# Kernel optimization log

Hardware: AMD Instinct MI355X
Metric: run time of the kernel (lower is better)

The kernel has to match this reference:

```python
import jax, jax.numpy as jnp
import numpy as np

D, d, s, n = 2048, 64, 32, 65536


def setup_inputs() -> dict:
    key = jax.random.key(0)
    k1, k2, k3, k4 = jax.random.split(key, 4)
    c = jax.random.normal(k1, (D, 1), dtype=jnp.float32)
    # torch parametrizations.orthogonal keeps Q.weight orthonormal-column; emulate via QR
    Q_raw = jax.random.normal(k2, (D, d + s), dtype=jnp.float32)
    Q, _ = jnp.linalg.qr(Q_raw)  # (D, d+s) orthonormal columns
    phi = jax.random.normal(k3, (d, n), dtype=jnp.float32)
    theta = jax.random.normal(k4, (d * (d + 1) // 2, s), dtype=jnp.float32)
    return {"c": c, "Q": Q, "phi": phi, "theta": theta}


def calculate_psi(phi):
    # vectorized upper-triangular outer product: rows ordered (0,0),(0,1),...,(0,d-1),(1,1),...
    dd = phi.shape[0]
    ii, jj = jnp.triu_indices(dd)  # matches the torch double loop ordering
    return phi[ii] * phi[jj]  # (d*(d+1)//2, n)


def reference(c, Q, phi, theta):
    psi = calculate_psi(phi)                       # (d(d+1)/2, n)
    quad = theta.T @ psi                           # (s, n)
    z = jnp.concatenate([phi, quad], axis=0)       # (d+s, n)
    return c + Q @ z                               # (D, n)
```

## Files before the change

### kernel.cpp

```cpp
#include <hip/hip_runtime.h>


__global__ __launch_bounds__(128) void quad_kernel(
    const float* __restrict__ phi,
    const float* __restrict__ theta,
    float* __restrict__ quad,
    const int n)
{
    __shared__ float ph[64][128];
    const int tid = threadIdx.x;
    const int colbase = blockIdx.x * 128;
    const int shalf = blockIdx.y;

    #pragma unroll
    for (int t = 0; t < 64; ++t) {
        const int e = t * 128 + tid;
        const int i = e >> 7;
        const int cc = e & 127;
        ph[i][cc] = phi[(size_t)i * n + colbase + cc];
    }
    __syncthreads();

    const float* __restrict__ th = theta + shalf * 16;

    float acc[16];
    #pragma unroll
    for (int ss = 0; ss < 16; ++ss) acc[ss] = 0.f;

    const float* __restrict__ tk = th;
    for (int i = 0; i < 64; ++i) {
        const float pi = ph[i][tid];
        for (int j = i; j < 64; ++j) {
            const float psi = pi * ph[j][tid];
            #pragma unroll
            for (int ss = 0; ss < 16; ++ss)
                acc[ss] = fmaf(tk[ss], psi, acc[ss]);
            tk += 32;
        }
    }

    const int col = colbase + tid;
    #pragma unroll
    for (int ss = 0; ss < 16; ++ss)
        quad[(size_t)(shalf * 16 + ss) * n + col] = acc[ss];
}

__global__ __launch_bounds__(256) void out_kernel(
    const float* __restrict__ cvec,
    const float* __restrict__ Q,
    const float* __restrict__ phi,
    const float* __restrict__ quad,
    float* __restrict__ out,
    const int n)
{
    __shared__ float Qt[96 * 64];
    __shared__ float Zs[96 * 64];
    const int tid = threadIdx.x;
    const int rowbase = blockIdx.x * 64;
    const int colbase = blockIdx.y * 64;

    {
        const int r = tid >> 2;
        const int kg = (tid & 3) * 24;
        const float* qp = Q + (size_t)(rowbase + r) * 96 + kg;
        #pragma unroll
        for (int t = 0; t < 6; ++t) {
            const float4 v = *(const float4*)(qp + t * 4);
            const int k0 = kg + t * 4;
            Qt[(k0 + 0) * 64 + r] = v.x;
            Qt[(k0 + 1) * 64 + r] = v.y;
            Qt[(k0 + 2) * 64 + r] = v.z;
            Qt[(k0 + 3) * 64 + r] = v.w;
        }
    }
    #pragma unroll
    for (int t = 0; t < 6; ++t) {
        const int q = t * 256 + tid;
        const int k = q >> 4;
        const int c4 = (q & 15) * 4;
        const float* src = (k < 64) ? (phi + (size_t)k * n)
                                    : (quad + (size_t)(k - 64) * n);
        *(float4*)&Zs[k * 64 + c4] = *(const float4*)(src + colbase + c4);
    }
    __syncthreads();

    const int cg = tid & 15;
    const int rg = tid >> 4;
    const int c0 = cg * 4;
    const int r0 = rg * 4;

    float acc[16];
    #pragma unroll
    for (int t = 0; t < 16; ++t) acc[t] = 0.f;

    #pragma unroll 8
    for (int k = 0; k < 96; ++k) {
        const float4 a = *(const float4*)&Qt[k * 64 + r0];
        const float4 b = *(const float4*)&Zs[k * 64 + c0];
        acc[0]  = fmaf(a.x, b.x, acc[0]);
        acc[1]  = fmaf(a.x, b.y, acc[1]);
        acc[2]  = fmaf(a.x, b.z, acc[2]);
        acc[3]  = fmaf(a.x, b.w, acc[3]);
        acc[4]  = fmaf(a.y, b.x, acc[4]);
        acc[5]  = fmaf(a.y, b.y, acc[5]);
        acc[6]  = fmaf(a.y, b.z, acc[6]);
        acc[7]  = fmaf(a.y, b.w, acc[7]);
        acc[8]  = fmaf(a.z, b.x, acc[8]);
        acc[9]  = fmaf(a.z, b.y, acc[9]);
        acc[10] = fmaf(a.z, b.z, acc[10]);
        acc[11] = fmaf(a.z, b.w, acc[11]);
        acc[12] = fmaf(a.w, b.x, acc[12]);
        acc[13] = fmaf(a.w, b.y, acc[13]);
        acc[14] = fmaf(a.w, b.z, acc[14]);
        acc[15] = fmaf(a.w, b.w, acc[15]);
    }

    #pragma unroll
    for (int i = 0; i < 4; ++i) {
        const int row = rowbase + r0 + i;
        const float cv = cvec[row];
        float4 v;
        v.x = acc[i * 4 + 0] + cv;
        v.y = acc[i * 4 + 1] + cv;
        v.z = acc[i * 4 + 2] + cv;
        v.w = acc[i * 4 + 3] + cv;
        *(float4*)&out[(size_t)row * n + colbase + c0] = v;
    }
}

extern "C" void kernel_launch(void* const* d_in, const int* in_sizes, int n_in,
                              void* d_out, int out_size, void* d_ws, size_t ws_size,
                              hipStream_t stream) {
    const float* c     = (const float*)d_in[0];
    const float* Q     = (const float*)d_in[1];
    const float* phi   = (const float*)d_in[2];
    const float* theta = (const float*)d_in[3];
    float* out  = (float*)d_out;
    float* quad = (float*)d_ws;

    const int D = in_sizes[0];
    const int n = in_sizes[2] / 64;

    quad_kernel<<<dim3(n / 128, 2), 128, 0, stream>>>(phi, theta, quad, n);
    out_kernel<<<dim3(D / 64, n / 64), 256, 0, stream>>>(c, Q, phi, quad, out, n);
}
```

Before: 1.014 ms.

## Use split-bf16 MFMA for output GEMM with transposed Z layout and async LDS loads

The fp32 FMA GEMM in the output kernel is replaced by bf16 MFMA 16x16x32 instructions using a hi/lo split (three products per pair) to approximate fp32 accuracy. A new prep kernel splits Q into bf16 hi/lo. The quad kernel now writes phi and quad together as a column-major Z in bf16 hi/lo. The output kernel loads its tiles with global_load_lds and uses a larger column tile. This targets the output GEMM's ALU and LDS cost, at the price of extra conversion work, a bigger workspace, and slightly lower precision from dropping the lo*lo term.

```diff
diff --git a/kernel.cpp b/kernel.cpp
--- a/kernel.cpp
+++ b/kernel.cpp
@@ -1,10 +1,45 @@
 #include <hip/hip_runtime.h>
 
+
+typedef short bf16x8 __attribute__((ext_vector_type(8)));
+typedef float f32x4 __attribute__((ext_vector_type(4)));
+typedef unsigned short u16;
+typedef unsigned int u32;
+
+__device__ inline u16 f2bf_rn(float x) {
+    u32 u = __float_as_uint(x);
+    return (u16)((u + 0x7FFFu + ((u >> 16) & 1u)) >> 16);
+}
+__device__ inline float bf2f(u16 h) { return __uint_as_float((u32)h << 16); }
+__device__ inline void bsplit(float x, u16& h, u16& l) {
+    h = f2bf_rn(x);
+    l = f2bf_rn(x - bf2f(h));
+}
+
+__device__ inline void gload_lds16(const void* g, void* l) {
+    __builtin_amdgcn_global_load_lds(
+        (const __attribute__((address_space(1))) void*)g,
+        (__attribute__((address_space(3))) void*)l,
+        16, 0, 0);
+}
+
+__global__ __launch_bounds__(256) void qprep_kernel(
+    const float* __restrict__ Q, u16* __restrict__ qh, u16* __restrict__ ql,
+    const int total)
+{
+    const int e = blockIdx.x * 256 + threadIdx.x;
+    if (e < total) {
+        u16 h, l;
+        bsplit(Q[e], h, l);
+        qh[e] = h;
+        ql[e] = l;
+    }
+}
 
 __global__ __launch_bounds__(128) void quad_kernel(
     const float* __restrict__ phi,
     const float* __restrict__ theta,
-    float* __restrict__ quad,
+    u16* __restrict__ zh, u16* __restrict__ zl,
     const int n)
 {
     __shared__ float ph[64][128];
@@ -21,13 +56,11 @@
     }
     __syncthreads();
 
-    const float* __restrict__ th = theta + shalf * 16;
-
     float acc[16];
     #pragma unroll
     for (int ss = 0; ss < 16; ++ss) acc[ss] = 0.f;
 
-    const float* __restrict__ tk = th;
+    const float* __restrict__ tk = theta + shalf * 16;
     for (int i = 0; i < 64; ++i) {
         const float pi = ph[i][tid];
         for (int j = i; j < 64; ++j) {
@@ -39,92 +72,113 @@
         }
     }
 
-    const int col = colbase + tid;
-    #pragma unroll
-    for (int ss = 0; ss < 16; ++ss)
-        quad[(size_t)(shalf * 16 + ss) * n + col] = acc[ss];
+    const int c = colbase + tid;
+    const size_t rb = (size_t)c * 96;
+
+    {
+        bf16x8 vh0, vh1, vl0, vl1;
+        #pragma unroll
+        for (int j = 0; j < 8; ++j) {
+            u16 h, l;
+            bsplit(acc[j], h, l);     vh0[j] = (short)h; vl0[j] = (short)l;
+            bsplit(acc[8 + j], h, l); vh1[j] = (short)h; vl1[j] = (short)l;
+        }
+        const size_t base = rb + 64 + shalf * 16;
+        *(bf16x8*)&zh[base] = vh0;
+        *(bf16x8*)&zh[base + 8] = vh1;
+        *(bf16x8*)&zl[base] = vl0;
+        *(bf16x8*)&zl[base + 8] = vl1;
+    }
+
+    if (shalf == 0) {
+        #pragma unroll
+        for (int ib = 0; ib < 64; ib += 8) {
+            bf16x8 vh, vl;
+            #pragma unroll
+            for (int j = 0; j < 8; ++j) {
+                u16 h, l;
+                bsplit(ph[ib + j][tid], h, l);
+                vh[j] = (short)h;
+                vl[j] = (short)l;
+            }
+            *(bf16x8*)&zh[rb + ib] = vh;
+            *(bf16x8*)&zl[rb + ib] = vl;
+        }
+    }
 }
 
 __global__ __launch_bounds__(256) void out_kernel(
     const float* __restrict__ cvec,
-    const float* __restrict__ Q,
-    const float* __restrict__ phi,
-    const float* __restrict__ quad,
-    float* __restrict__ out,
-    const int n)
+    const u16* __restrict__ qh, const u16* __restrict__ ql,
+    const u16* __restrict__ zh, const u16* __restrict__ zl,
+    float* __restrict__ out, const int n)
 {
-    __shared__ float Qt[96 * 64];
-    __shared__ float Zs[96 * 64];
+    __shared__ u16 lds[36864];
     const int tid = threadIdx.x;
+    const int lane = tid & 63;
+    const int wid = tid >> 6;
     const int rowbase = blockIdx.x * 64;
-    const int colbase = blockIdx.y * 64;
+    const int colbase = blockIdx.y * 128;
 
     {
-        const int r = tid >> 2;
-        const int kg = (tid & 3) * 24;
-        const float* qp = Q + (size_t)(rowbase + r) * 96 + kg;
-        #pragma unroll
-        for (int t = 0; t < 6; ++t) {
-            const float4 v = *(const float4*)(qp + t * 4);
-            const int k0 = kg + t * 4;
-            Qt[(k0 + 0) * 64 + r] = v.x;
-            Qt[(k0 + 1) * 64 + r] = v.y;
-            Qt[(k0 + 2) * 64 + r] = v.z;
-            Qt[(k0 + 3) * 64 + r] = v.w;
-        }
-    }
-    #pragma unroll
-    for (int t = 0; t < 6; ++t) {
-        const int q = t * 256 + tid;
-        const int k = q >> 4;
-        const int c4 = (q & 15) * 4;
-        const float* src = (k < 64) ? (phi + (size_t)k * n)
-                                    : (quad + (size_t)(k - 64) * n);
-        *(float4*)&Zs[k * 64 + c4] = *(const float4*)(src + colbase + c4);
+        const char* gq_h = (const char*)(qh + (size_t)rowbase * 96) + lane * 16;
+        const char* gq_l = (const char*)(ql + (size_t)rowbase * 96) + lane * 16;
+        const char* gz_h = (const char*)(zh + (size_t)colbase * 96) + lane * 16;
+        const char* gz_l = (const char*)(zl + (size_t)colbase * 96) + lane * 16;
+        char* lb = (char*)&lds[0];
+        for (int jc = wid; jc < 12; jc += 4) {
+            gload_lds16(gq_h + jc * 1024, lb + jc * 1024);
+            gload_lds16(gq_l + jc * 1024, lb + 12288 + jc * 1024);
+        }
+        for (int jc = wid; jc < 24; jc += 4) {
+            gload_lds16(gz_h + jc * 1024, lb + 24576 + jc * 1024);
+            gload_lds16(gz_l + jc * 1024, lb + 49152 + jc * 1024);
+        }
     }
     __syncthreads();
 
-    const int cg = tid & 15;
-    const int rg = tid >> 4;
-    const int c0 = cg * 4;
-    const int r0 = rg * 4;
-
-    float acc[16];
-    #pragma unroll
-    for (int t = 0; t < 16; ++t) acc[t] = 0.f;
-
-    #pragma unroll 8
-    for (int k = 0; k < 96; ++k) {
-        const float4 a = *(const float4*)&Qt[k * 64 + r0];
-        const float4 b = *(const float4*)&Zs[k * 64 + c0];
-        acc[0]  = fmaf(a.x, b.x, acc[0]);
-        acc[1]  = fmaf(a.x, b.y, acc[1]);
-        acc[2]  = fmaf(a.x, b.z, acc[2]);
-        acc[3]  = fmaf(a.x, b.w, acc[3]);
-        acc[4]  = fmaf(a.y, b.x, acc[4]);
-        acc[5]  = fmaf(a.y, b.y, acc[5]);
-        acc[6]  = fmaf(a.y, b.z, acc[6]);
-        acc[7]  = fmaf(a.y, b.w, acc[7]);
-        acc[8]  = fmaf(a.z, b.x, acc[8]);
-        acc[9]  = fmaf(a.z, b.y, acc[9]);
-        acc[10] = fmaf(a.z, b.z, acc[10]);
-        acc[11] = fmaf(a.z, b.w, acc[11]);
-        acc[12] = fmaf(a.w, b.x, acc[12]);
-        acc[13] = fmaf(a.w, b.y, acc[13]);
-        acc[14] = fmaf(a.w, b.z, acc[14]);
-        acc[15] = fmaf(a.w, b.w, acc[15]);
-    }
-
-    #pragma unroll
-    for (int i = 0; i < 4; ++i) {
-        const int row = rowbase + r0 + i;
-        const float cv = cvec[row];
-        float4 v;
-        v.x = acc[i * 4 + 0] + cv;
-        v.y = acc[i * 4 + 1] + cv;
-        v.z = acc[i * 4 + 2] + cv;
-        v.w = acc[i * 4 + 3] + cv;
-        *(float4*)&out[(size_t)row * n + colbase + c0] = v;
+    f32x4 acc[4][2] = {};
+    const int ar = lane & 15;
+    const int ag = lane >> 4;
+    const int wc0 = wid * 32;
+
+    #pragma unroll
+    for (int ks = 0; ks < 3; ++ks) {
+        const int ko = ks * 32 + ag * 8;
+        bf16x8 bh[2], bl[2];
+        #pragma unroll
+        for (int nf = 0; nf < 2; ++nf) {
+            const int c = wc0 + nf * 16 + ar;
+            bh[nf] = *(const bf16x8*)&lds[12288 + c * 96 + ko];
+            bl[nf] = *(const bf16x8*)&lds[24576 + c * 96 + ko];
+        }
+        #pragma unroll
+        for (int m = 0; m < 4; ++m) {
+            const int r = m * 16 + ar;
+            const bf16x8 ahf = *(const bf16x8*)&lds[r * 96 + ko];
+            const bf16x8 alf = *(const bf16x8*)&lds[6144 + r * 96 + ko];
+            #pragma unroll
+            for (int nf = 0; nf < 2; ++nf) {
+                acc[m][nf] = __builtin_amdgcn_mfma_f32_16x16x32_bf16(ahf, bh[nf], acc[m][nf], 0, 0, 0);
+                acc[m][nf] = __builtin_amdgcn_mfma_f32_16x16x32_bf16(ahf, bl[nf], acc[m][nf], 0, 0, 0);
+                acc[m][nf] = __builtin_amdgcn_mfma_f32_16x16x32_bf16(alf, bh[nf], acc[m][nf], 0, 0, 0);
+            }
+        }
+    }
+
+    const int r4 = (lane >> 4) * 4;
+    #pragma unroll
+    for (int m = 0; m < 4; ++m) {
+        const int rb = rowbase + m * 16 + r4;
+        #pragma unroll
+        for (int j = 0; j < 4; ++j) {
+            const float cv = cvec[rb + j];
+            #pragma unroll
+            for (int nf = 0; nf < 2; ++nf) {
+                const int cc = colbase + wc0 + nf * 16 + (lane & 15);
+                out[(size_t)(rb + j) * n + cc] = acc[m][nf][j] + cv;
+            }
+        }
     }
 }
 
@@ -135,12 +189,17 @@
     const float* Q     = (const float*)d_in[1];
     const float* phi   = (const float*)d_in[2];
     const float* theta = (const float*)d_in[3];
-    float* out  = (float*)d_out;
-    float* quad = (float*)d_ws;
+    float* out = (float*)d_out;
 
     const int D = in_sizes[0];
     const int n = in_sizes[2] / 64;
 
-    quad_kernel<<<dim3(n / 128, 2), 128, 0, stream>>>(phi, theta, quad, n);
-    out_kernel<<<dim3(D / 64, n / 64), 256, 0, stream>>>(c, Q, phi, quad, out, n);
-}
+    u16* zh = (u16*)d_ws;
+    u16* zl = (u16*)((char*)d_ws + (size_t)n * 192);
+    u16* qh = (u16*)((char*)d_ws + (size_t)n * 384);
+    u16* ql = (u16*)((char*)d_ws + (size_t)n * 384 + (size_t)D * 192);
+
+    qprep_kernel<<<(D * 96 + 255) / 256, 256, 0, stream>>>(Q, qh, ql, D * 96);
+    quad_kernel<<<dim3(n / 128, 2), 128, 0, stream>>>(phi, theta, zh, zl, n);
+    out_kernel<<<dim3(D / 64, n / 128), 256, 0, stream>>>(c, qh, ql, zh, zl, out, n);
+}
```

Result: faster. 870.4 us (-14.2%).
